# Kernel tuning notes

Hardware: AMD Instinct MI355X
Metric: run time of the kernel (lower is better)

Reference implementation:

```python
import jax, jax.numpy as jnp
import numpy as np

B, T, MED, LAB, GLU, D = 1024, 25, 145, 1956, 16, 64
H = D // 2  # 32


def _gat(h, adj, w, a):
    # h: [B, MED, 1] drug-usage counts; in_features=1 so Wh = h * w
    Wh = h * w  # [B, MED, D]
    f1 = Wh @ a[:D]  # [B, MED]
    f2 = Wh @ a[D:]  # [B, MED]
    e = jax.nn.leaky_relu(f1[:, :, None] + f2[:, None, :], 0.2)  # [B, MED, MED]
    e = jnp.where(adj > 0, e, jnp.float32(-9e15))
    attn = jax.nn.softmax(e, axis=-1)
    return jax.nn.elu(attn @ Wh)  # [B, MED, D]


def _mha(q, k, v, wq, wk, wv, wo, nh=4):
    Bq, Lq, Dm = q.shape
    dh = Dm // nh
    qh = (q @ wq).reshape(Bq, Lq, nh, dh)
    kh = (k @ wk).reshape(Bq, k.shape[1], nh, dh)
    vh = (v @ wv).reshape(Bq, v.shape[1], nh, dh)
    s = jnp.einsum('bqhd,bkhd->bhqk', qh, kh) / np.float32(np.sqrt(dh))
    a = jax.nn.softmax(s, axis=-1)
    o = jnp.einsum('bhqk,bkhd->bqhd', a, vh).reshape(Bq, Lq, Dm)
    return o @ wo


def _gated(x, g):
    # Attn_encoder: per-position gated emphasis, preserves sequence shape
    return x * jax.nn.sigmoid(x @ g)[..., None]


def setup_inputs():
    key = jax.random.key(0)
    ks = jax.random.split(key, 40)
    n = lambda i, shape, s=0.05: (jax.random.normal(ks[i], shape, dtype=jnp.float32) * s)
    inp = {
        'lab': jax.random.normal(ks[0], (B, LAB), dtype=jnp.float32),
        'glu': jax.random.normal(ks[1], (B, T, GLU), dtype=jnp.float32),
        'time_feat': jax.random.uniform(ks[2], (B, T, GLU), dtype=jnp.float32),
        'med': jax.random.uniform(ks[3], (B, T, MED), dtype=jnp.float32),
        'ehr_adj': (jax.random.uniform(ks[4], (MED, MED)) > 0.9).astype(jnp.float32),
        'ddi_adj': (jax.random.uniform(ks[5], (MED, MED)) > 0.9).astype(jnp.float32),
        'time_adj': (jax.random.uniform(ks[6], (MED, MED)) > 0.9).astype(jnp.float32),
        'sll_w1': n(7, (LAB, D)), 'sll_b1': n(8, (D,)),
        'sll_w2': n(9, (D, H)), 'sll_b2': n(10, (H,)),
        'glu_w': n(11, (2 * GLU, H)), 'glu_b': n(12, (H,)), 'glu_gate': n(13, (H,)),
        'med_w': n(14, (MED, D)), 'med_b': n(15, (D,)), 'med_gate': n(16, (D,)),
        'gat_ehr_w': n(17, (D,)), 'gat_ehr_a': n(18, (2 * D,)),
        'gat_time_w': n(19, (D,)), 'gat_time_a': n(20, (2 * D,)),
        'gat_ddi_w': n(21, (D,)), 'gat_ddi_a': n(22, (2 * D,)),
        'ga_wq': n(23, (D, D)), 'ga_wk': n(24, (D, D)), 'ga_wv': n(25, (D, D)), 'ga_wo': n(26, (D, D)),
        'm1_wq': n(27, (D, D)), 'm1_wk': n(28, (D, D)), 'm1_wv': n(29, (D, D)), 'm1_wo': n(30, (D, D)),
        'm2_wq': n(31, (D, D)), 'm2_wk': n(32, (D, D)), 'm2_wv': n(33, (D, D)), 'm2_wo': n(34, (D, D)),
        'out_w1': n(35, (MED * D, MED * D // 8), 0.01), 'out_b1': n(36, (MED * D // 8,)),
        'out_w2': n(37, (MED * D // 8, MED)), 'out_b2': n(38, (MED,)),
    }
    return inp


def reference(lab, glu, time_feat, med, ehr_adj, ddi_adj, time_adj,
              sll_w1, sll_b1, sll_w2, sll_b2,
              glu_w, glu_b, glu_gate, med_w, med_b, med_gate,
              gat_ehr_w, gat_ehr_a, gat_time_w, gat_time_a, gat_ddi_w, gat_ddi_a,
              ga_wq, ga_wk, ga_wv, ga_wo,
              m1_wq, m1_wk, m1_wv, m1_wo,
              m2_wq, m2_wk, m2_wv, m2_wo,
              out_w1, out_b1, out_w2, out_b2):
    relu = jax.nn.relu
    medb = (med > 0.9).astype(med.dtype)  # multi-hot medication history
    # static_ll, repeated over visits
    static = relu(relu(lab @ sll_w1 + sll_b1) @ sll_w2 + sll_b2)  # [B, H]
    static_seq = jnp.broadcast_to(static[:, None, :], (B, T, H))
    # per-patient drug usage counts over past visits
    h = jnp.sum(medb[:, :-1], axis=1)[..., None]  # [B, MED, 1]
    g_ehr = _gat(h, ehr_adj, gat_ehr_w, gat_ehr_a)
    g_time = _gat(h, time_adj, gat_time_w, gat_time_a)
    g_ddi = _gat(h, ddi_adj, gat_ddi_w, gat_ddi_a)
    all_graph = jnp.concatenate([g_ehr, g_time, g_ddi], axis=1)  # [B, 3*MED, D]
    dm = _mha(all_graph, all_graph, all_graph, ga_wq, ga_wk, ga_wv, ga_wo)
    drug_mem = dm.reshape(B, 3, MED, D).mean(axis=1)  # [B, MED, D]
    # medication / glucose encoders
    med_rep = _gated(medb[:, :-1] @ med_w + med_b, med_gate)  # [B, T-1, D]
    glu_in = jnp.concatenate([glu, time_feat], axis=-1)  # [B, T, 2*GLU]
    glu_rep = _gated(jnp.tanh(glu_in @ glu_w + glu_b), glu_gate)  # [B, T, H]
    patient = jnp.concatenate([glu_rep, static_seq], axis=-1)  # [B, T, D]
    # m1: query = med history, keys/values = patient visits
    E_en = _mha(med_rep, patient, patient, m1_wq, m1_wk, m1_wv, m1_wo)  # [B, T-1, D]
    e0 = E_en[:, :1]  # [B, 1, D]
    # m2: query = drug memory, keys/values = encoded state
    E_de = _mha(drug_mem, e0, e0, m2_wq, m2_wk, m2_wv, m2_wo)  # [B, MED, D]
    final = E_de.reshape(B, MED * D)
    hid = relu(relu(final) @ out_w1 + out_b1)
    return hid @ out_w2 + out_b2  # [B, MED]
```

## Files before the change

kernel.cpp:

```cpp
#include <hip/hip_runtime.h>
#include <math.h>

#define B_   1024
#define T_   25
#define MED_ 145
#define LAB_ 1956
#define GLU_ 16
#define D_   64
#define H_   32
#define HID_ 1160
#define KC_  978
#define OUTN_ (B_ * MED_)
#define W1N_ (D_ * HID_)

__global__ __launch_bounds__(512) void k_pre(
    const float* __restrict__ lab, const float* __restrict__ sw1,
    const float* __restrict__ out_w1,
    const float* __restrict__ wo, const float* __restrict__ m2wv,
    const float* __restrict__ m2wo,
    float* __restrict__ part, float* __restrict__ w1c, float* __restrict__ W3) {
  __shared__ float smem[7824];
  const int tid = threadIdx.x;
  const int bid = blockIdx.x;
  if (bid < 256) {
    const int b0 = (bid >> 1) * 8;
    const int kc = bid & 1;
    const int k0 = kc * KC_;
    float* lab_f = smem;
    for (int e = tid; e < 8 * 489; e += 512) {
      int r = e / 489, i = e - r * 489;
      float2 v = ((const float2*)(lab + (size_t)(b0 + r) * LAB_ + k0))[i];
      lab_f[r * 978 + 2 * i] = v.x;
      lab_f[r * 978 + 2 * i + 1] = v.y;
    }
    __syncthreads();
    const int col = tid & 63;
    const int slice = tid >> 6;
    float acc[8] = {0.f, 0.f, 0.f, 0.f, 0.f, 0.f, 0.f, 0.f};
    #pragma unroll 2
    for (int k = slice; k < KC_; k += 8) {
      float w = sw1[(size_t)(k0 + k) * D_ + col];
      #pragma unroll
      for (int r = 0; r < 8; ++r) acc[r] = fmaf(lab_f[r * 978 + k], w, acc[r]);
    }
    __syncthreads();
    float* red = smem;
    #pragma unroll
    for (int r = 0; r < 8; ++r) red[(r * 8 + slice) * 64 + col] = acc[r];
    __syncthreads();
    {
      int r = tid >> 6, d = tid & 63;
      float v = 0.f;
      #pragma unroll
      for (int s2 = 0; s2 < 8; ++s2) v += red[(r * 8 + s2) * 64 + d];
      part[(size_t)kc * B_ * D_ + (size_t)(b0 + r) * D_ + d] = v;
    }
  } else if (bid < 836) {
    const int b2 = bid - 256;
    const int i = tid & 127;
    const int msl = tid >> 7;
    const int idx = b2 * 128 + i;
    const int m0 = (msl * MED_) >> 2, m1 = ((msl + 1) * MED_) >> 2;
    const float* p = out_w1 + idx + (size_t)m0 * W1N_;
    float s = 0.f;
    #pragma unroll 4
    for (int m = m0; m < m1; ++m) {
      s += *p;
      p += (size_t)W1N_;
    }
    float* red = smem;
    red[msl * 128 + i] = s;
    __syncthreads();
    if (tid < 128)
      w1c[b2 * 128 + tid] = red[tid] + red[128 + tid] + red[256 + tid] + red[384 + tid];
  } else {
    float* tmp = smem;
    for (int e = tid; e < 4096; e += 512) {
      int i = e >> 6, j = e & 63;
      float s = 0.f;
      #pragma unroll 8
      for (int k = 0; k < 64; ++k) s = fmaf(wo[i * 64 + k], m2wv[k * 64 + j], s);
      tmp[e] = s;
    }
    __syncthreads();
    for (int e = tid; e < 4096; e += 512) {
      int i = e >> 6, j = e & 63;
      float s = 0.f;
      #pragma unroll 8
      for (int k = 0; k < 64; ++k) s = fmaf(tmp[i * 64 + k], m2wo[k * 64 + j], s);
      W3[e] = s;
    }
  }
}

__global__ __launch_bounds__(256) void k_perb(
    const float* __restrict__ glu, const float* __restrict__ tf,
    const float* __restrict__ med, const float* __restrict__ part,
    const float* __restrict__ sb1, const float* __restrict__ sw2,
    const float* __restrict__ sb2,
    const float* __restrict__ glu_w, const float* __restrict__ glu_b,
    const float* __restrict__ glu_gate, const float* __restrict__ med_w,
    const float* __restrict__ med_b, const float* __restrict__ med_gate,
    const float* __restrict__ wq, const float* __restrict__ wk,
    const float* __restrict__ wv, const float* __restrict__ W3,
    float* __restrict__ rr) {
  const int b = blockIdx.x;
  const int tid = threadIdx.x;
  const int d = tid & 63;
  const int s4 = tid >> 6;
  __shared__ float xin_s[T_][2 * GLU_];
  __shared__ float y_s[T_][H_];
  __shared__ float gate_s[T_];
  __shared__ float medrow_s[160];
  __shared__ float t1_s[D_];
  __shared__ float st_s[H_];
  __shared__ float pat_s[28][D_];
  __shared__ float q0_s[D_];
  __shared__ float kh_s[T_][D_];
  __shared__ float vh_s[T_][D_];
  __shared__ float at_s[4][T_];
  __shared__ float o_s[D_];
  __shared__ float vec_s[D_];
  __shared__ float red4[4][D_];

  for (int e = tid; e < T_ * GLU_; e += 256) {
    int t = e >> 4, i = e & 15;
    xin_s[t][i] = glu[((size_t)b * T_ + t) * GLU_ + i];
    xin_s[t][GLU_ + i] = tf[((size_t)b * T_ + t) * GLU_ + i];
  }
  if (tid < MED_) medrow_s[tid] = med[(size_t)b * T_ * MED_ + tid];
  if (tid >= 192) {
    int dd = tid - 192;
    size_t o = (size_t)b * D_ + dd;
    t1_s[dd] = fmaxf(part[o] + part[(size_t)B_ * D_ + o] + sb1[dd], 0.f);
  }
  __syncthreads();

  for (int e = tid; e < T_ * H_; e += 256) {
    int t = e >> 5, j = e & 31;
    float s = glu_b[j];
    #pragma unroll 8
    for (int i = 0; i < 2 * GLU_; ++i) s = fmaf(xin_s[t][i], glu_w[i * H_ + j], s);
    y_s[t][j] = tanhf(s);
  }
  if (tid >= 224) {
    int j = tid - 224;
    float s = sb2[j];
    #pragma unroll 8
    for (int dd = 0; dd < D_; ++dd) s = fmaf(t1_s[dd], sw2[dd * H_ + j], s);
    st_s[j] = fmaxf(s, 0.f);
  }
  __syncthreads();

  {
    float x = 0.f;
    for (int m = s4; m < MED_; m += 4)
      if (medrow_s[m] > 0.9f) x += med_w[m * D_ + d];
    red4[s4][d] = x;
  }
  if (tid < 8 * T_) {
    int t = tid >> 3, sl = tid & 7;
    float s = 0.f;
    #pragma unroll
    for (int i = 0; i < 4; ++i) {
      int j = sl * 4 + i;
      s = fmaf(y_s[t][j], glu_gate[j], s);
    }
    s += __shfl_xor(s, 1);
    s += __shfl_xor(s, 2);
    s += __shfl_xor(s, 4);
    if (sl == 0) gate_s[t] = 1.f / (1.f + __expf(-s));
  }
  __syncthreads();

  if (tid < D_) {
    float x = med_b[tid] + red4[0][tid] + red4[1][tid] + red4[2][tid] + red4[3][tid];
    float v = x * med_gate[tid];
    #pragma unroll
    for (int off = 32; off > 0; off >>= 1) v += __shfl_xor(v, off);
    q0_s[tid] = x * (1.f / (1.f + __expf(-v)));
  }
  for (int e = tid; e < 28 * H_; e += 256) {
    int t = e >> 5, j = e & 31;
    if (t < T_) {
      pat_s[t][j] = y_s[t][j] * gate_s[t];
      pat_s[t][H_ + j] = st_s[j];
    } else {
      pat_s[t][j] = 0.f;
      pat_s[t][H_ + j] = 0.f;
    }
  }
  __syncthreads();

  {
    float aK[7] = {0.f, 0.f, 0.f, 0.f, 0.f, 0.f, 0.f};
    float aV[7] = {0.f, 0.f, 0.f, 0.f, 0.f, 0.f, 0.f};
    #pragma unroll 4
    for (int j = 0; j < D_; ++j) {
      float wkj = wk[j * D_ + d];
      float wvj = wv[j * D_ + d];
      #pragma unroll
      for (int i = 0; i < 7; ++i) {
        float p = pat_s[s4 + 4 * i][j];
        aK[i] = fmaf(p, wkj, aK[i]);
        aV[i] = fmaf(p, wvj, aV[i]);
      }
    }
    #pragma unroll
    for (int i = 0; i < 7; ++i) {
      int t = s4 + 4 * i;
      if (t < T_) { kh_s[t][d] = aK[i]; vh_s[t][d] = aV[i]; }
    }
  }
  {
    float qp = 0.f;
    #pragma unroll
    for (int i = 0; i < 16; ++i) {
      int j = s4 * 16 + i;
      qp = fmaf(q0_s[j], wq[j * D_ + d], qp);
    }
    red4[s4][d] = qp;
  }
  __syncthreads();

  if (tid < D_) vec_s[tid] = red4[0][tid] + red4[1][tid] + red4[2][tid] + red4[3][tid];
  __syncthreads();

  if (tid < 128) {
    int h = tid >> 5, t = tid & 31;
    bool valid = t < T_;
    float sc = -3.4e38f;
    if (valid) {
      float a = 0.f;
      #pragma unroll
      for (int i = 0; i < 16; ++i) a = fmaf(vec_s[h * 16 + i], kh_s[t][h * 16 + i], a);
      sc = a * 0.25f;
    }
    float m = sc;
    #pragma unroll
    for (int off = 16; off > 0; off >>= 1) m = fmaxf(m, __shfl_xor(m, off, 32));
    float e = valid ? __expf(sc - m) : 0.f;
    float sum = e;
    #pragma unroll
    for (int off = 16; off > 0; off >>= 1) sum += __shfl_xor(sum, off, 32);
    if (valid) at_s[h][t] = e / sum;
  }
  __syncthreads();

  if (tid < D_) {
    int h = tid >> 4;
    float s = 0.f;
    #pragma unroll
    for (int t = 0; t < T_; ++t) s = fmaf(at_s[h][t], vh_s[t][tid], s);
    o_s[tid] = s;
  }
  __syncthreads();

  {
    float p = 0.f;
    #pragma unroll
    for (int i = 0; i < 16; ++i) {
      int j = s4 * 16 + i;
      p = fmaf(o_s[j], W3[j * D_ + d], p);
    }
    red4[s4][d] = p;
  }
  __syncthreads();

  if (tid < D_) {
    float v = red4[0][tid] + red4[1][tid] + red4[2][tid] + red4[3][tid];
    rr[(size_t)b * D_ + tid] = fmaxf(v, 0.f);
  }
}

__global__ __launch_bounds__(640) void k_final(
    const float* __restrict__ rr, const float* __restrict__ w1c,
    const float* __restrict__ b1, const float* __restrict__ w2,
    float* __restrict__ p4) {
  const int tid = threadIdx.x;
  const int b0 = blockIdx.x * 16;
  const int jq = blockIdx.y;
  const int j0 = jq * 290;
  __shared__ float rr_s[16][D_];
  __shared__ float hid_s[16][292];
  for (int e = tid; e < 16 * D_; e += 640)
    ((float*)rr_s)[e] = rr[(size_t)b0 * D_ + e];
  __syncthreads();
  if (tid < 580) {
    int jj = tid % 290, rh = tid / 290;
    const float* wp = w1c + (size_t)(j0 + jj);
    float bb = b1[j0 + jj];
    float acc[8] = {0.f, 0.f, 0.f, 0.f, 0.f, 0.f, 0.f, 0.f};
    #pragma unroll 4
    for (int d4 = 0; d4 < 16; ++d4) {
      float w0 = wp[(size_t)(4 * d4 + 0) * HID_];
      float w1v = wp[(size_t)(4 * d4 + 1) * HID_];
      float w2v = wp[(size_t)(4 * d4 + 2) * HID_];
      float w3v = wp[(size_t)(4 * d4 + 3) * HID_];
      #pragma unroll
      for (int r8 = 0; r8 < 8; ++r8) {
        float4 rv = *(const float4*)&rr_s[rh * 8 + r8][4 * d4];
        acc[r8] += rv.x * w0 + rv.y * w1v + rv.z * w2v + rv.w * w3v;
      }
    }
    #pragma unroll
    for (int r8 = 0; r8 < 8; ++r8)
      hid_s[rh * 8 + r8][jj] = fmaxf(acc[r8] + bb, 0.f);
  }
  __syncthreads();
  if (tid < 464) {
    int ng = tid >> 4;
    int r  = tid & 15;
    const float* w2p = w2 + (size_t)j0 * MED_ + ng * 5;
    float a0 = 0.f, a1 = 0.f, a2 = 0.f, a3 = 0.f, a4 = 0.f;
    #pragma unroll 2
    for (int k = 0; k < 290; ++k) {
      float h = hid_s[r][k];
      const float* wkp = w2p + (size_t)k * MED_;
      a0 = fmaf(h, wkp[0], a0);
      a1 = fmaf(h, wkp[1], a1);
      a2 = fmaf(h, wkp[2], a2);
      a3 = fmaf(h, wkp[3], a3);
      a4 = fmaf(h, wkp[4], a4);
    }
    float* dst = p4 + (size_t)jq * OUTN_ + (size_t)(b0 + r) * MED_ + ng * 5;
    dst[0] = a0; dst[1] = a1; dst[2] = a2; dst[3] = a3; dst[4] = a4;
  }
}

__global__ __launch_bounds__(256) void k_combine(
    const float* __restrict__ p4, const float* __restrict__ b2,
    float* __restrict__ out) {
  int idx = blockIdx.x * 256 + threadIdx.x;
  int n = idx - (idx / MED_) * MED_;
  out[idx] = p4[idx] + p4[OUTN_ + idx] + p4[2 * OUTN_ + idx] +
             p4[3 * OUTN_ + idx] + b2[n];
}

extern "C" void kernel_launch(void* const* d_in, const int* in_sizes, int n_in,
                              void* d_out, int out_size, void* d_ws, size_t ws_size,
                              hipStream_t stream) {
  (void)in_sizes; (void)n_in; (void)out_size; (void)ws_size;
  const float* lab      = (const float*)d_in[0];
  const float* glu      = (const float*)d_in[1];
  const float* tf       = (const float*)d_in[2];
  const float* med      = (const float*)d_in[3];
  const float* sll_w1   = (const float*)d_in[7];
  const float* sll_b1   = (const float*)d_in[8];
  const float* sll_w2   = (const float*)d_in[9];
  const float* sll_b2   = (const float*)d_in[10];
  const float* glu_w    = (const float*)d_in[11];
  const float* glu_b    = (const float*)d_in[12];
  const float* glu_gate = (const float*)d_in[13];
  const float* med_w    = (const float*)d_in[14];
  const float* med_b    = (const float*)d_in[15];
  const float* med_gate = (const float*)d_in[16];
  const float* m1_wq    = (const float*)d_in[27];
  const float* m1_wk    = (const float*)d_in[28];
  const float* m1_wv    = (const float*)d_in[29];
  const float* m1_wo    = (const float*)d_in[30];
  const float* m2_wv    = (const float*)d_in[33];
  const float* m2_wo    = (const float*)d_in[34];
  const float* out_w1   = (const float*)d_in[35];
  const float* out_b1   = (const float*)d_in[36];
  const float* out_w2   = (const float*)d_in[37];
  const float* out_b2   = (const float*)d_in[38];
  float* out = (float*)d_out;

  float* ws   = (float*)d_ws;
  float* part = ws;
  float* w1c  = part + 2 * B_ * D_;
  float* rr   = w1c + W1N_;
  float* W3   = rr + B_ * D_;
  float* p4   = W3 + D_ * D_;

  hipLaunchKernelGGL(k_pre, dim3(837), dim3(512), 0, stream,
                     lab, sll_w1, out_w1, m1_wo, m2_wv, m2_wo, part, w1c, W3);
  hipLaunchKernelGGL(k_perb, dim3(B_), dim3(256), 0, stream,
                     glu, tf, med, part, sll_b1, sll_w2, sll_b2,
                     glu_w, glu_b, glu_gate, med_w, med_b, med_gate,
                     m1_wq, m1_wk, m1_wv, W3, rr);
  hipLaunchKernelGGL(k_final, dim3(B_ / 16, 4), dim3(640), 0, stream,
                     rr, w1c, out_b1, out_w2, p4);
  hipLaunchKernelGGL(k_combine, dim3(OUTN_ / 256), dim3(256), 0, stream,
                     p4, out_b2, out);
}
```

Baseline: 289.6 us.

## Stage out_w2 chunks in shared memory with register-prefetch double buffering

The second GEMM in k_final used to read w2 straight from global memory through strided per-thread loads. It now copies w2 in 29-row chunks into shared memory, prefetching the next chunk into registers while the current one is consumed. The thread mapping changes to one output column per thread over 4 batch rows, so each thread's global writes are coalesced. This adds extra barriers per chunk, about 17KB more shared memory and 7 prefetch registers per thread, which may lower occupancy.

```diff
diff --git a/kernel.cpp b/kernel.cpp
--- a/kernel.cpp
+++ b/kernel.cpp
@@ -283,8 +283,18 @@
   const int j0 = jq * 290;
   __shared__ float rr_s[16][D_];
   __shared__ float hid_s[16][292];
+  __shared__ float w2t[29 * MED_];
   for (int e = tid; e < 16 * D_; e += 640)
     ((float*)rr_s)[e] = rr[(size_t)b0 * D_ + e];
+  float pre[7];
+  {
+    const float* src = w2 + (size_t)j0 * MED_;
+    #pragma unroll
+    for (int i = 0; i < 7; ++i) {
+      int e = tid + i * 640;
+      pre[i] = (e < 29 * MED_) ? src[e] : 0.f;
+    }
+  }
   __syncthreads();
   if (tid < 580) {
     int jj = tid % 290, rh = tid / 290;
@@ -307,24 +317,46 @@
     for (int r8 = 0; r8 < 8; ++r8)
       hid_s[rh * 8 + r8][jj] = fmaxf(acc[r8] + bb, 0.f);
   }
-  __syncthreads();
-  if (tid < 464) {
-    int ng = tid >> 4;
-    int r  = tid & 15;
-    const float* w2p = w2 + (size_t)j0 * MED_ + ng * 5;
-    float a0 = 0.f, a1 = 0.f, a2 = 0.f, a3 = 0.f, a4 = 0.f;
-    #pragma unroll 2
-    for (int k = 0; k < 290; ++k) {
-      float h = hid_s[r][k];
-      const float* wkp = w2p + (size_t)k * MED_;
-      a0 = fmaf(h, wkp[0], a0);
-      a1 = fmaf(h, wkp[1], a1);
-      a2 = fmaf(h, wkp[2], a2);
-      a3 = fmaf(h, wkp[3], a3);
-      a4 = fmaf(h, wkp[4], a4);
-    }
-    float* dst = p4 + (size_t)jq * OUTN_ + (size_t)(b0 + r) * MED_ + ng * 5;
-    dst[0] = a0; dst[1] = a1; dst[2] = a2; dst[3] = a3; dst[4] = a4;
+  const int n = tid % MED_, rg = tid / MED_;
+  float a0 = 0.f, a1 = 0.f, a2 = 0.f, a3 = 0.f;
+  for (int c = 0; c < 10; ++c) {
+    __syncthreads();
+    #pragma unroll
+    for (int i = 0; i < 7; ++i) {
+      int e = tid + i * 640;
+      if (e < 29 * MED_) w2t[e] = pre[i];
+    }
+    __syncthreads();
+    if (c < 9) {
+      const float* src = w2 + (size_t)(j0 + (c + 1) * 29) * MED_;
+      #pragma unroll
+      for (int i = 0; i < 7; ++i) {
+        int e = tid + i * 640;
+        pre[i] = (e < 29 * MED_) ? src[e] : 0.f;
+      }
+    }
+    if (tid < 580) {
+      const float* hp0 = &hid_s[rg * 4 + 0][c * 29];
+      const float* hp1 = &hid_s[rg * 4 + 1][c * 29];
+      const float* hp2 = &hid_s[rg * 4 + 2][c * 29];
+      const float* hp3 = &hid_s[rg * 4 + 3][c * 29];
+      const float* wt = w2t + n;
+      #pragma unroll
+      for (int k = 0; k < 29; ++k) {
+        float wv = wt[k * MED_];
+        a0 = fmaf(hp0[k], wv, a0);
+        a1 = fmaf(hp1[k], wv, a1);
+        a2 = fmaf(hp2[k], wv, a2);
+        a3 = fmaf(hp3[k], wv, a3);
+      }
+    }
+  }
+  if (tid < 580) {
+    float* dst = p4 + (size_t)jq * OUTN_ + (size_t)(b0 + rg * 4) * MED_ + n;
+    dst[0 * MED_] = a0;
+    dst[1 * MED_] = a1;
+    dst[2 * MED_] = a2;
+    dst[3 * MED_] = a3;
   }
 }
 
```

Measured after the change: 245.0 us. 1.18x faster.
